# Kernel tuning notes

Measured on AMD Instinct MI355X. Metric: run time of the kernel, lower is better.

Reference implementation:

```python
import jax, jax.numpy as jnp
import numpy as np

D = 64        # gat_output_dim == state_dim
HID = 128     # hidden_dim
ADIM = 2 * D  # action_dim (ope_dim + insert_dim)


def _mk(key, shape, scale=0.05):
    return jax.random.normal(key, shape, dtype=jnp.float32) * scale


def setup_inputs() -> dict:
    key = jax.random.key(0)
    ks = jax.random.split(key, 24)
    inp = {
        "ope_gat": jax.random.normal(ks[0], (8, 258, D), jnp.float32),
        "insert_gat": jax.random.normal(ks[1], (8, 256, D), jnp.float32),
        "h": jax.random.normal(ks[2], (8, D), jnp.float32),
        "c": jax.random.normal(ks[3], (8, D), jnp.float32),
        # LSTM (pytorch layout: gates i,f,g,o stacked -> [4D, in])
        "W_ih": _mk(ks[4], (4 * D, D)),
        "W_hh": _mk(ks[5], (4 * D, D)),
        "b_ih": _mk(ks[6], (4 * D,)),
        "b_hh": _mk(ks[7], (4 * D,)),
        # V_net: Linear(D,HID) -> Linear(HID,HID) -> LeakyReLU -> Linear(HID,1)
        "Wv0": _mk(ks[8], (HID, D)), "bv0": _mk(ks[9], (HID,)),
        "Wv1": _mk(ks[10], (HID, HID)), "bv1": _mk(ks[11], (HID,)),
        "Wv2": _mk(ks[12], (1, HID)), "bv2": _mk(ks[13], (1,)),
        # A_net: Linear(D+ADIM,HID) -> Linear(HID,HID) -> LeakyReLU -> Linear(HID,1)
        "Wa0": _mk(ks[14], (HID, D + ADIM)), "ba0": _mk(ks[15], (HID,)),
        "Wa1": _mk(ks[16], (HID, HID)), "ba1": _mk(ks[17], (HID,)),
        "Wa2": _mk(ks[18], (1, HID)), "ba2": _mk(ks[19], (1,)),
    }
    return inp


def _lrelu(x):
    return jnp.where(x >= 0, x, 0.01 * x)


def _forward(ope_gat, insert_gat, h, c,
             W_ih, W_hh, b_ih, b_hh,
             Wv0, bv0, Wv1, bv1, Wv2, bv2,
             Wa0, ba0, Wa1, ba1, Wa2, ba2):
    ope = ope_gat[:, 1:-1]                # [B, O, D]
    state = ope.mean(axis=-2)             # [B, D]

    # single-step LSTM (pytorch gate order i, f, g, o)
    gates = state @ W_ih.T + b_ih + h @ W_hh.T + b_hh  # [B, 4D]
    i_g, f_g, g_g, o_g = jnp.split(gates, 4, axis=-1)
    cn = jax.nn.sigmoid(f_g) * c + jax.nn.sigmoid(i_g) * jnp.tanh(g_g)
    hn = jax.nn.sigmoid(o_g) * jnp.tanh(cn)
    rnn_state = hn                        # [B, D]

    # V head (note: no activation after first linear -- name-overwrite bug)
    V = _lrelu((rnn_state @ Wv0.T + bv0) @ Wv1.T + bv1) @ Wv2.T + bv2  # [B, 1]

    # A head on the full (ope x insert) cross-join; ope side is detached.
    ope_d = jax.lax.stop_gradient(ope)    # [B, O, D]
    B, O, _ = ope_d.shape
    I = insert_gat.shape[1]
    # Decompose first linear over the concat [state | ope | insert] (exact math).
    Ws, Wo, Wi = Wa0[:, :D], Wa0[:, D:2 * D], Wa0[:, 2 * D:]
    h0 = (rnn_state @ Ws.T)[:, None, None, :] \
         + jnp.einsum('bod,hd->boh', ope_d, Wo)[:, :, None, :] \
         + jnp.einsum('bid,hd->bih', insert_gat, Wi)[:, None, :, :] \
         + ba0                              # [B, O, I, HID]
    h1 = _lrelu(jnp.einsum('boih,gh->boig', h0, Wa1) + ba1)
    A = (jnp.einsum('boih,h->boi', h1, Wa2[0]) + ba2[0]).reshape(B, O * I)
    return V, A, hn, cn


def reference(ope_gat, insert_gat, h, c,
              W_ih, W_hh, b_ih, b_hh,
              Wv0, bv0, Wv1, bv1, Wv2, bv2,
              Wa0, ba0, Wa1, ba1, Wa2, ba2):
    return _forward(ope_gat, insert_gat, h, c,
                    W_ih, W_hh, b_ih, b_hh,
                    Wv0, bv0, Wv1, bv1, Wv2, bv2,
                    Wa0, ba0, Wa1, ba1, Wa2, ba2)
```

## Files before the change

### kernel.cpp

```cpp
#include <hip/hip_runtime.h>
#include <hip/hip_bf16.h>
#include <math.h>

typedef unsigned short u16;

#define FB    524288
#define SOFF  26896
#define C1S   27920

__device__ __forceinline__ u16 f2b(float x) { __hip_bfloat16 b = __float2bfloat16(x); return *(u16*)&b; }
__device__ __forceinline__ void cvt8(const uint4 u, float* f) {
    f[0] = __uint_as_float(u.x << 16); f[1] = __uint_as_float(u.x & 0xFFFF0000u);
    f[2] = __uint_as_float(u.y << 16); f[3] = __uint_as_float(u.y & 0xFFFF0000u);
    f[4] = __uint_as_float(u.z << 16); f[5] = __uint_as_float(u.z & 0xFFFF0000u);
    f[6] = __uint_as_float(u.w << 16); f[7] = __uint_as_float(u.w & 0xFFFF0000u);
}
__device__ __forceinline__ float dot4(const float4 a, const float4 b) {
    return a.x*b.x + a.y*b.y + a.z*b.z + a.w*b.w;
}

__global__ __launch_bounds__(256) void k12_main(
    const float* __restrict__ ope, const float* __restrict__ ins,
    const float* __restrict__ hin, const float* __restrict__ cin,
    const float* __restrict__ W_ih, const float* __restrict__ W_hh,
    const float* __restrict__ b_ih, const float* __restrict__ b_hh,
    const float* __restrict__ Wv0, const float* __restrict__ bv0,
    const float* __restrict__ Wv1, const float* __restrict__ bv1,
    const float* __restrict__ Wv2, const float* __restrict__ bv2,
    const float* __restrict__ Wa0, const float* __restrict__ ba0,
    const float* __restrict__ Wa1, const float* __restrict__ ba1,
    const float* __restrict__ Wa2, const float* __restrict__ ba2,
    float* __restrict__ ws)
{
    __shared__ __align__(16) u16 Wa1s[128*136];
    __shared__ __align__(16) u16 Wsel[128*72];
    __shared__ __align__(16) u16 inrows[16*72];
    __shared__ __align__(16) float P[16*132];
    const int t = threadIdx.x;

    if (blockIdx.x < 256) {
        const int b = blockIdx.x >> 5;
        const int r0 = (blockIdx.x & 31) * 16;
        const int side = (r0 >= 256) ? 1 : 0;

        #pragma unroll
        for (int k = 0; k < 16; ++k) {
            const int e4 = t + k*256;
            const int g = e4 >> 5, hq = (e4 & 31) * 4;
            const float4 w = *(const float4*)(Wa1 + g*128 + hq);
            ushort4 u; u.x = f2b(w.x); u.y = f2b(w.y); u.z = f2b(w.z); u.w = f2b(w.w);
            *(ushort4*)&Wa1s[g*136 + hq] = u;
        }
        #pragma unroll
        for (int k = 0; k < 8; ++k) {
            const int e4 = t + k*256;
            const int h = e4 >> 4, dq = (e4 & 15) * 4;
            const float4 w = *(const float4*)(Wa0 + h*192 + 64 + side*64 + dq);
            ushort4 u; u.x = f2b(w.x); u.y = f2b(w.y); u.z = f2b(w.z); u.w = f2b(w.w);
            *(ushort4*)&Wsel[h*72 + dq] = u;
        }
        {
            const int r = t >> 4, dq = (t & 15) * 4;
            const float* src = side
                ? (ins + b*16384 + (r0 - 256 + r)*64 + dq)
                : (ope + b*16512 + (1 + r0 + r)*64 + dq);
            const float4 w = *(const float4*)src;
            ushort4 u; u.x = f2b(w.x); u.y = f2b(w.y); u.z = f2b(w.z); u.w = f2b(w.w);
            *(ushort4*)&inrows[r*72 + dq] = u;
        }
        __syncthreads();

        const int r = t >> 4;
        const int q = t & 15;

        {
            float acc[8] = {0.f,0.f,0.f,0.f,0.f,0.f,0.f,0.f};
            #pragma unroll
            for (int d8 = 0; d8 < 64; d8 += 8) {
                float iv[8];
                cvt8(*(const uint4*)&inrows[r*72 + d8], iv);
                #pragma unroll
                for (int k = 0; k < 8; ++k) {
                    float wv[8];
                    cvt8(*(const uint4*)&Wsel[(q + 16*k)*72 + d8], wv);
                    #pragma unroll
                    for (int j = 0; j < 8; ++j) acc[k] += wv[j] * iv[j];
                }
            }
            #pragma unroll
            for (int k = 0; k < 8; ++k) P[r*132 + q + 16*k] = acc[k];
        }
        __syncthreads();

        {
            float acc[8] = {0.f,0.f,0.f,0.f,0.f,0.f,0.f,0.f};
            #pragma unroll
            for (int h8 = 0; h8 < 128; h8 += 8) {
                const float4 p0 = *(const float4*)&P[r*132 + h8];
                const float4 p1 = *(const float4*)&P[r*132 + h8 + 4];
                #pragma unroll
                for (int k = 0; k < 8; ++k) {
                    float wv[8];
                    cvt8(*(const uint4*)&Wa1s[(q + 16*k)*136 + h8], wv);
                    float a = acc[k];
                    a += wv[0]*p0.x + wv[1]*p0.y + wv[2]*p0.z + wv[3]*p0.w;
                    a += wv[4]*p1.x + wv[5]*p1.y + wv[6]*p1.z + wv[7]*p1.w;
                    acc[k] = a;
                }
            }
            float part = 0.f;
            const int row = side ? (b*256 + r0 - 256 + r) : (b*256 + r0 + r);
            float* dst = side ? (ws + 262144 + row*128) : (ws + row*128);
            #pragma unroll
            for (int k = 0; k < 8; ++k) {
                const int g = q + 16*k;
                part = fmaf(0.505f * Wa2[g], acc[k], part);
                dst[g] = acc[k];
            }
            part += __shfl_xor(part, 1);
            part += __shfl_xor(part, 2);
            part += __shfl_xor(part, 4);
            part += __shfl_xor(part, 8);
            if (q == 0) {
                if (!side) ws[FB + 2320 + row] = part;
                else       ws[FB + 4368 + row] = part;
            }
        }
    } else {
        const int b = blockIdx.x - 256;
        float* f = (float*)Wa1s;
        float* state = f;
        float* hvec  = f + 64;
        float* gl    = f + 128;
        float* hn_s  = f + 384;
        float* t0a   = f + 448;
        float* t1a   = f + 576;
        float* s2s   = f + 704;
        float* red   = f + 832;

        {
            const int d = t & 63, q = t >> 6;
            const float* p = ope + b*16512 + (1 + q*64)*64 + d;
            float s = 0.f;
            #pragma unroll 8
            for (int r = 0; r < 64; ++r) s += p[r*64];
            red[t] = s;
        }
        __syncthreads();
        if (t < 64)       state[t]   = (red[t] + red[t+64] + red[t+128] + red[t+192]) * (1.f/256.f);
        else if (t < 128) hvec[t-64] = hin[b*64 + (t-64)];
        __syncthreads();

        {
            float g = b_ih[t] + b_hh[t];
            const float4* wi = (const float4*)(W_ih + t*64);
            const float4* wh = (const float4*)(W_hh + t*64);
            #pragma unroll
            for (int k = 0; k < 16; ++k)
                g += dot4(wi[k], *(const float4*)&state[k*4])
                   + dot4(wh[k], *(const float4*)&hvec[k*4]);
            gl[t] = g;
        }
        __syncthreads();

        if (t < 64) {
            const float ig = gl[t], fg = gl[64+t], gg = gl[128+t], og = gl[192+t];
            const float c  = cin[b*64 + t];
            const float si = 1.f/(1.f + expf(-ig));
            const float sf = 1.f/(1.f + expf(-fg));
            const float so = 1.f/(1.f + expf(-og));
            const float cn = sf*c + si*tanhf(gg);
            const float hn = so*tanhf(cn);
            ws[FB + 1288 + b*64 + t] = hn;
            ws[FB + 1800 + b*64 + t] = cn;
            hn_s[t] = hn;
        }
        __syncthreads();

        if (t < 128) {
            float a = bv0[t];
            const float4* w = (const float4*)(Wv0 + t*64);
            #pragma unroll
            for (int k = 0; k < 16; ++k) a += dot4(w[k], *(const float4*)&hn_s[k*4]);
            t0a[t] = a;
        }
        __syncthreads();
        if (t < 128) {
            float a = bv1[t];
            const float4* w = (const float4*)(Wv1 + t*128);
            #pragma unroll
            for (int k = 0; k < 32; ++k) a += dot4(w[k], *(const float4*)&t0a[k*4]);
            a = (a >= 0.f) ? a : 0.01f*a;
            t1a[t] = a * Wv2[t];
            float s2 = ba0[t];
            const float4* w0 = (const float4*)(Wa0 + t*192);
            #pragma unroll
            for (int k = 0; k < 16; ++k) s2 += dot4(w0[k], *(const float4*)&hn_s[k*4]);
            s2s[t] = s2;
        }
        __syncthreads();
        if (t < 128) {
            float sv = ba1[t];
            const float4* w = (const float4*)(Wa1 + t*128);
            #pragma unroll
            for (int k = 0; k < 32; ++k) sv += dot4(w[k], *(const float4*)&s2s[k*4]);
            ws[FB + SOFF + b*128 + t] = sv;
            red[t] = 0.505f * Wa2[t] * sv;
        }
        __syncthreads();
        if (t < 64) {
            float c = red[t] + red[t + 64];
            float v = t1a[t] + t1a[t + 64];
            c += __shfl_xor(c, 32); v += __shfl_xor(v, 32);
            c += __shfl_xor(c, 16); v += __shfl_xor(v, 16);
            c += __shfl_xor(c, 8);  v += __shfl_xor(v, 8);
            c += __shfl_xor(c, 4);  v += __shfl_xor(v, 4);
            c += __shfl_xor(c, 2);  v += __shfl_xor(v, 2);
            c += __shfl_xor(c, 1);  v += __shfl_xor(v, 1);
            if (t == 0) {
                ws[FB + C1S + b]  = c + ba2[0];
                ws[FB + 1280 + b] = v + bv2[0];
            }
        }
    }
}

__global__ __launch_bounds__(256) void k3_adv(const float* __restrict__ ws,
                                              const float* __restrict__ Wa2,
                                              float* __restrict__ out)
{
    const int t = threadIdx.x;
    const int b = blockIdx.x >> 6;
    const int o0 = (blockIdx.x & 63) * 4;

    float acc[4] = {0.f, 0.f, 0.f, 0.f};
    #pragma unroll
    for (int gc = 0; gc < 8; ++gc) {
        float syv[16], wv[16];
        {
            const float* yr = ws + 262144 + (b*256 + t)*128 + gc*16;
            const float* sr = ws + FB + SOFF + b*128 + gc*16;
            const float* wr = Wa2 + gc*16;
            #pragma unroll
            for (int k = 0; k < 4; ++k) {
                const float4 y4 = *(const float4*)(yr + k*4);
                const float4 s4 = *(const float4*)(sr + k*4);
                const float4 w4 = *(const float4*)(wr + k*4);
                syv[k*4+0] = y4.x + s4.x; syv[k*4+1] = y4.y + s4.y;
                syv[k*4+2] = y4.z + s4.z; syv[k*4+3] = y4.w + s4.w;
                wv[k*4+0] = 0.495f*w4.x; wv[k*4+1] = 0.495f*w4.y;
                wv[k*4+2] = 0.495f*w4.z; wv[k*4+3] = 0.495f*w4.w;
            }
        }
        #pragma unroll
        for (int o = 0; o < 4; ++o) {
            const float* xr = ws + (b*256 + o0 + o)*128 + gc*16;
            float a = acc[o];
            #pragma unroll
            for (int k = 0; k < 4; ++k) {
                const float4 x4 = *(const float4*)(xr + k*4);
                a = fmaf(wv[k*4+0], fabsf(x4.x + syv[k*4+0]), a);
                a = fmaf(wv[k*4+1], fabsf(x4.y + syv[k*4+1]), a);
                a = fmaf(wv[k*4+2], fabsf(x4.z + syv[k*4+2]), a);
                a = fmaf(wv[k*4+3], fabsf(x4.w + syv[k*4+3]), a);
            }
            acc[o] = a;
        }
    }
    const float c2  = ws[FB + 4368 + b*256 + t];
    const float c1s = ws[FB + C1S + b];
    #pragma unroll
    for (int o = 0; o < 4; ++o)
        out[8 + b*65536 + (o0 + o)*256 + t] =
            ws[FB + 2320 + b*256 + o0 + o] + c1s + c2 + acc[o];

    if (blockIdx.x == 0) {
        if (t < 8) out[t] = ws[FB + 1280 + t];
        #pragma unroll
        for (int j = t; j < 512; j += 256) {
            out[524296 + j] = ws[FB + 1288 + j];
            out[524808 + j] = ws[FB + 1800 + j];
        }
    }
}

extern "C" void kernel_launch(void* const* d_in, const int* in_sizes, int n_in,
                              void* d_out, int out_size, void* d_ws, size_t ws_size,
                              hipStream_t stream) {
    float* ws = (float*)d_ws;
    float* out = (float*)d_out;

    k12_main<<<dim3(264), dim3(256), 0, stream>>>(
        (const float*)d_in[0], (const float*)d_in[1],
        (const float*)d_in[2], (const float*)d_in[3],
        (const float*)d_in[4], (const float*)d_in[5],
        (const float*)d_in[6], (const float*)d_in[7],
        (const float*)d_in[8], (const float*)d_in[9],
        (const float*)d_in[10], (const float*)d_in[11],
        (const float*)d_in[12], (const float*)d_in[13],
        (const float*)d_in[14], (const float*)d_in[15],
        (const float*)d_in[16], (const float*)d_in[17],
        (const float*)d_in[18], (const float*)d_in[19], ws);
    k3_adv  <<<dim3(512), dim3(256), 0, stream>>>(ws, (const float*)d_in[18], out);
}
```

Baseline: 124.5 us.

## Use MFMA bf16 for projection GEMMs, split adv kernel over hidden halves

Replaces the scalar bf16→fp32 dot-product loops in the row-projection blocks with MFMA 16x16x32 bf16 instructions for both the Wsel and Wa1 GEMMs. The intermediate P is now stored as bf16, and the per-row partial sums are reduced across waves through shared memory. The LSTM-side mean reduction now uses float4 loads over more row groups. The k3_adv kernel doubles its grid by splitting the hidden dimension across two half-blocks that combine through shared memory. This adds another bf16 rounding of the intermediate and an extra sync in exchange for better parallelism.

```diff
diff --git a/kernel.cpp b/kernel.cpp
--- a/kernel.cpp
+++ b/kernel.cpp
@@ -3,18 +3,14 @@
 #include <math.h>
 
 typedef unsigned short u16;
+typedef short short8 __attribute__((ext_vector_type(8)));
+typedef float f32x4 __attribute__((ext_vector_type(4)));
 
 #define FB    524288
 #define SOFF  26896
 #define C1S   27920
 
 __device__ __forceinline__ u16 f2b(float x) { __hip_bfloat16 b = __float2bfloat16(x); return *(u16*)&b; }
-__device__ __forceinline__ void cvt8(const uint4 u, float* f) {
-    f[0] = __uint_as_float(u.x << 16); f[1] = __uint_as_float(u.x & 0xFFFF0000u);
-    f[2] = __uint_as_float(u.y << 16); f[3] = __uint_as_float(u.y & 0xFFFF0000u);
-    f[4] = __uint_as_float(u.z << 16); f[5] = __uint_as_float(u.z & 0xFFFF0000u);
-    f[6] = __uint_as_float(u.w << 16); f[7] = __uint_as_float(u.w & 0xFFFF0000u);
-}
 __device__ __forceinline__ float dot4(const float4 a, const float4 b) {
     return a.x*b.x + a.y*b.y + a.z*b.z + a.w*b.w;
 }
@@ -35,7 +31,8 @@
     __shared__ __align__(16) u16 Wa1s[128*136];
     __shared__ __align__(16) u16 Wsel[128*72];
     __shared__ __align__(16) u16 inrows[16*72];
-    __shared__ __align__(16) float P[16*132];
+    __shared__ __align__(16) u16 Pb[16*136];
+    __shared__ float partb[64];
     const int t = threadIdx.x;
 
     if (blockIdx.x < 256) {
@@ -70,61 +67,73 @@
         }
         __syncthreads();
 
-        const int r = t >> 4;
-        const int q = t & 15;
-
-        {
-            float acc[8] = {0.f,0.f,0.f,0.f,0.f,0.f,0.f,0.f};
-            #pragma unroll
-            for (int d8 = 0; d8 < 64; d8 += 8) {
-                float iv[8];
-                cvt8(*(const uint4*)&inrows[r*72 + d8], iv);
-                #pragma unroll
-                for (int k = 0; k < 8; ++k) {
-                    float wv[8];
-                    cvt8(*(const uint4*)&Wsel[(q + 16*k)*72 + d8], wv);
-                    #pragma unroll
-                    for (int j = 0; j < 8; ++j) acc[k] += wv[j] * iv[j];
-                }
-            }
-            #pragma unroll
-            for (int k = 0; k < 8; ++k) P[r*132 + q + 16*k] = acc[k];
-        }
-        __syncthreads();
-
-        {
-            float acc[8] = {0.f,0.f,0.f,0.f,0.f,0.f,0.f,0.f};
-            #pragma unroll
-            for (int h8 = 0; h8 < 128; h8 += 8) {
-                const float4 p0 = *(const float4*)&P[r*132 + h8];
-                const float4 p1 = *(const float4*)&P[r*132 + h8 + 4];
-                #pragma unroll
-                for (int k = 0; k < 8; ++k) {
-                    float wv[8];
-                    cvt8(*(const uint4*)&Wa1s[(q + 16*k)*136 + h8], wv);
-                    float a = acc[k];
-                    a += wv[0]*p0.x + wv[1]*p0.y + wv[2]*p0.z + wv[3]*p0.w;
-                    a += wv[4]*p1.x + wv[5]*p1.y + wv[6]*p1.z + wv[7]*p1.w;
-                    acc[k] = a;
-                }
-            }
-            float part = 0.f;
-            const int row = side ? (b*256 + r0 - 256 + r) : (b*256 + r0 + r);
-            float* dst = side ? (ws + 262144 + row*128) : (ws + row*128);
-            #pragma unroll
-            for (int k = 0; k < 8; ++k) {
-                const int g = q + 16*k;
-                part = fmaf(0.505f * Wa2[g], acc[k], part);
-                dst[g] = acc[k];
-            }
-            part += __shfl_xor(part, 1);
-            part += __shfl_xor(part, 2);
-            part += __shfl_xor(part, 4);
-            part += __shfl_xor(part, 8);
-            if (q == 0) {
-                if (!side) ws[FB + 2320 + row] = part;
-                else       ws[FB + 4368 + row] = part;
-            }
+        const int lane = t & 63;
+        const int wv   = t >> 6;
+        const int lrow = lane & 15;
+        const int grp  = lane >> 4;
+        const int lk   = grp * 8;
+
+        const short8 a0 = *(const short8*)&inrows[lrow*72 + lk];
+        const short8 a1 = *(const short8*)&inrows[lrow*72 + 32 + lk];
+        #pragma unroll
+        for (int nt = 0; nt < 2; ++nt) {
+            const int h0 = (wv*2 + nt) * 16;
+            const short8 b0 = *(const short8*)&Wsel[(h0 + lrow)*72 + lk];
+            const short8 b1 = *(const short8*)&Wsel[(h0 + lrow)*72 + 32 + lk];
+            f32x4 acc = {0.f, 0.f, 0.f, 0.f};
+            acc = __builtin_amdgcn_mfma_f32_16x16x32_bf16(a0, b0, acc, 0, 0, 0);
+            acc = __builtin_amdgcn_mfma_f32_16x16x32_bf16(a1, b1, acc, 0, 0, 0);
+            #pragma unroll
+            for (int r = 0; r < 4; ++r)
+                Pb[(4*grp + r)*136 + h0 + lrow] = f2b(acc[r]);
+        }
+        __syncthreads();
+
+        short8 pa[4];
+        #pragma unroll
+        for (int ks = 0; ks < 4; ++ks)
+            pa[ks] = *(const short8*)&Pb[lrow*136 + ks*32 + lk];
+
+        const int rowbase = b*256 + r0 - side*256;
+        float* dst = side ? (ws + 262144) : ws;
+        float part[4] = {0.f, 0.f, 0.f, 0.f};
+        #pragma unroll
+        for (int nt = 0; nt < 2; ++nt) {
+            const int g0 = (wv*2 + nt) * 16;
+            f32x4 acc = {0.f, 0.f, 0.f, 0.f};
+            #pragma unroll
+            for (int ks = 0; ks < 4; ++ks) {
+                const short8 bb = *(const short8*)&Wa1s[(g0 + lrow)*136 + ks*32 + lk];
+                acc = __builtin_amdgcn_mfma_f32_16x16x32_bf16(pa[ks], bb, acc, 0, 0, 0);
+            }
+            const float wa = 0.505f * Wa2[g0 + lrow];
+            #pragma unroll
+            for (int r = 0; r < 4; ++r) {
+                const int m = 4*grp + r;
+                dst[(rowbase + m)*128 + g0 + lrow] = acc[r];
+                part[r] = fmaf(wa, acc[r], part[r]);
+            }
+        }
+        #pragma unroll
+        for (int r = 0; r < 4; ++r) {
+            float p = part[r];
+            p += __shfl_xor(p, 1);
+            p += __shfl_xor(p, 2);
+            p += __shfl_xor(p, 4);
+            p += __shfl_xor(p, 8);
+            part[r] = p;
+        }
+        if (lrow == 0) {
+            #pragma unroll
+            for (int r = 0; r < 4; ++r)
+                partb[wv*16 + grp*4 + r] = part[r];
+        }
+        __syncthreads();
+        if (t < 16) {
+            const float p = partb[t] + partb[16 + t] + partb[32 + t] + partb[48 + t];
+            const int row = rowbase + t;
+            if (!side) ws[FB + 2320 + row] = p;
+            else       ws[FB + 4368 + row] = p;
         }
     } else {
         const int b = blockIdx.x - 256;
@@ -137,18 +146,28 @@
         float* t1a   = f + 576;
         float* s2s   = f + 704;
         float* red   = f + 832;
+        float* red4  = f + 1024;
 
         {
-            const int d = t & 63, q = t >> 6;
-            const float* p = ope + b*16512 + (1 + q*64)*64 + d;
+            const int dq = (t & 15) * 4;
+            const int q  = t >> 4;
+            const float* p = ope + b*16512 + (1 + q)*64 + dq;
+            float4 s = make_float4(0.f, 0.f, 0.f, 0.f);
+            #pragma unroll
+            for (int r = 0; r < 16; ++r) {
+                const float4 v = *(const float4*)(p + r*1024);
+                s.x += v.x; s.y += v.y; s.z += v.z; s.w += v.w;
+            }
+            *(float4*)&red4[(q*16 + (t & 15))*4] = s;
+        }
+        __syncthreads();
+        if (t < 64) {
             float s = 0.f;
-            #pragma unroll 8
-            for (int r = 0; r < 64; ++r) s += p[r*64];
-            red[t] = s;
-        }
-        __syncthreads();
-        if (t < 64)       state[t]   = (red[t] + red[t+64] + red[t+128] + red[t+192]) * (1.f/256.f);
-        else if (t < 128) hvec[t-64] = hin[b*64 + (t-64)];
+            #pragma unroll
+            for (int q = 0; q < 16; ++q)
+                s += red4[(q*16 + (t >> 2))*4 + (t & 3)];
+            state[t] = s * (1.f/256.f);
+        } else if (t < 128) hvec[t-64] = hin[b*64 + (t-64)];
         __syncthreads();
 
         {
@@ -229,16 +248,23 @@
                                               const float* __restrict__ Wa2,
                                               float* __restrict__ out)
 {
+    __shared__ __align__(16) float cmb[128*4];
     const int t = threadIdx.x;
-    const int b = blockIdx.x >> 6;
-    const int o0 = (blockIdx.x & 63) * 4;
+    const int blk = blockIdx.x;
+    const int b  = blk >> 7;
+    const int o0 = ((blk >> 1) & 63) * 4;
+    const int ih = blk & 1;
+    const int gh = t >> 7;
+    const int li = t & 127;
+    const int i  = ih * 128 + li;
 
     float acc[4] = {0.f, 0.f, 0.f, 0.f};
     #pragma unroll
-    for (int gc = 0; gc < 8; ++gc) {
+    for (int gc2 = 0; gc2 < 4; ++gc2) {
+        const int gc = gh*4 + gc2;
         float syv[16], wv[16];
         {
-            const float* yr = ws + 262144 + (b*256 + t)*128 + gc*16;
+            const float* yr = ws + 262144 + (b*256 + i)*128 + gc*16;
             const float* sr = ws + FB + SOFF + b*128 + gc*16;
             const float* wr = Wa2 + gc*16;
             #pragma unroll
@@ -267,14 +293,20 @@
             acc[o] = a;
         }
     }
-    const float c2  = ws[FB + 4368 + b*256 + t];
-    const float c1s = ws[FB + C1S + b];
-    #pragma unroll
-    for (int o = 0; o < 4; ++o)
-        out[8 + b*65536 + (o0 + o)*256 + t] =
-            ws[FB + 2320 + b*256 + o0 + o] + c1s + c2 + acc[o];
-
-    if (blockIdx.x == 0) {
+    if (gh) *(float4*)&cmb[li*4] = make_float4(acc[0], acc[1], acc[2], acc[3]);
+    __syncthreads();
+    if (!gh) {
+        const float4 c4 = *(const float4*)&cmb[li*4];
+        acc[0] += c4.x; acc[1] += c4.y; acc[2] += c4.z; acc[3] += c4.w;
+        const float c2  = ws[FB + 4368 + b*256 + i];
+        const float c1s = ws[FB + C1S + b];
+        #pragma unroll
+        for (int o = 0; o < 4; ++o)
+            out[8 + b*65536 + (o0 + o)*256 + i] =
+                ws[FB + 2320 + b*256 + o0 + o] + c1s + c2 + acc[o];
+    }
+
+    if (blk == 0) {
         if (t < 8) out[t] = ws[FB + 1280 + t];
         #pragma unroll
         for (int j = t; j < 512; j += 256) {
@@ -301,5 +333,5 @@
         (const float*)d_in[14], (const float*)d_in[15],
         (const float*)d_in[16], (const float*)d_in[17],
         (const float*)d_in[18], (const float*)d_in[19], ws);
-    k3_adv  <<<dim3(512), dim3(256), 0, stream>>>(ws, (const float*)d_in[18], out);
+    k3_adv  <<<dim3(1024), dim3(256), 0, stream>>>(ws, (const float*)d_in[18], out);
 }
```

Measured after the change: 128.3 us. +3.1%, slower.
